# Kernel optimization log

Hardware: AMD Instinct MI355X
Metric: run time of the kernel (lower is better)

The kernel has to match this reference:

```python
import jax, jax.numpy as jnp
import numpy as np

EPS = 1e-5
GROUPS = 32


def _groupnorm(x, gamma, beta):
    B, C, H, W = x.shape
    xr = x.reshape(B, GROUPS, C // GROUPS, H, W)
    mu = xr.mean(axis=(2, 3, 4), keepdims=True)
    var = xr.var(axis=(2, 3, 4), keepdims=True)
    xn = ((xr - mu) * jax.lax.rsqrt(var + EPS)).reshape(B, C, H, W)
    return xn * gamma[None, :, None, None] + beta[None, :, None, None]


def _conv1x1(x, w, b):
    # x: [B,C,H,W], w: [Cout,Cin], b: [Cout]
    return jnp.einsum('bchw,oc->bohw', x, w) + b[None, :, None, None]


def setup_inputs() -> dict:
    key = jax.random.key(0)
    ks = jax.random.split(key, 11)
    B, C, H, W = 4, 64, 64, 64
    s = 0.05  # weight scale for well-conditioned softmax
    inp = {
        'x': jax.random.normal(ks[0], (B, C, H, W), jnp.float32),
        'gn_gamma': jnp.ones((C,), jnp.float32),
        'gn_beta': jnp.zeros((C,), jnp.float32),
        'wq': jax.random.normal(ks[1], (C, C), jnp.float32) * s,
        'bq': jnp.zeros((C,), jnp.float32),
        'wk': jax.random.normal(ks[2], (C, C), jnp.float32) * s,
        'bk': jnp.zeros((C,), jnp.float32),
        'wv': jax.random.normal(ks[3], (C, C), jnp.float32) * s,
        'bv': jnp.zeros((C,), jnp.float32),
        'wp': jax.random.normal(ks[4], (C, C), jnp.float32) * s,
        'bp': jnp.zeros((C,), jnp.float32),
    }
    return inp


def reference(x, gn_gamma, gn_beta, wq, bq, wk, bk, wv, bv, wp, bp):
    B, C, H, W = x.shape
    h = _groupnorm(x, gn_gamma, gn_beta)
    q = _conv1x1(h, wq, bq)
    k = _conv1x1(h, wk, bk)
    v = _conv1x1(h, wv, bv)
    # scores over all spatial positions: [B,H,W,H,W]
    scale = 1.0 / jnp.sqrt(jnp.asarray(C, x.dtype))
    w = jnp.einsum('bchw,bcHW->bhwHW', q, k) * scale
    w = jax.nn.softmax(w.reshape(B, H, W, H * W), axis=-1).reshape(B, H, W, H, W)
    h = jnp.einsum('bhwHW,bcHW->bchw', w, v)
    h = _conv1x1(h, wp, bp)
    return x + h
```

## Files before the change

kernel.cpp:

```cpp
#include <hip/hip_runtime.h>
#include <stdint.h>

#define Bn 4
#define Cn 64
#define Sn 4096
#define Gn 32

typedef float v4f __attribute__((ext_vector_type(4)));
typedef short v8s __attribute__((ext_vector_type(8)));
typedef short v4s __attribute__((ext_vector_type(4)));

#define MFMA16(a,b,c) __builtin_amdgcn_mfma_f32_16x16x32_bf16((a),(b),(c),0,0,0)

#define QSC 0.18033688011112042f

__device__ __forceinline__ float bf2f(uint16_t u){
  union { uint32_t i; float f; } x; x.i = ((uint32_t)u) << 16; return x.f;
}
__device__ __forceinline__ uint16_t f2bf(float f){
  union { float f; uint32_t i; } x; x.f = f;
  uint32_t r = x.i + 0x7fffu + ((x.i >> 16) & 1u);
  return (uint16_t)(r >> 16);
}
__device__ __forceinline__ uint32_t cvtpk(float a, float b){
  uint32_t r;
  asm("v_cvt_pk_bf16_f32 %0, %1, %2" : "=v"(r) : "v"(a), "v"(b));
  return r;
}

__global__ __launch_bounds__(256) void gn_stats(
    const float* __restrict__ x,
    const float* __restrict__ wq, const float* __restrict__ wk,
    const float* __restrict__ wv, const float* __restrict__ wp,
    float* __restrict__ stats, uint16_t* __restrict__ Wbf)
{
  const int tid = threadIdx.x;
  if (blockIdx.x >= 128) {
    const int m = blockIdx.x - 128;
    const float* src = (m == 0) ? wq : (m == 1) ? wk : (m == 2) ? wv : wp;
    const float sc  = (m == 0) ? QSC : 1.f;
    uint16_t* dst = Wbf + (m << 12);
    #pragma unroll
    for (int i = 0; i < 4; ++i) {
      const int e = (tid << 4) + (i << 2);
      float4 v = *(const float4*)(src + e);
      v4s o;
      o[0] = (short)f2bf(v.x*sc); o[1] = (short)f2bf(v.y*sc);
      o[2] = (short)f2bf(v.z*sc); o[3] = (short)f2bf(v.w*sc);
      *(v4s*)(dst + e) = o;
    }
    return;
  }
  const float* base = x + (size_t)blockIdx.x * 8192;
  float sum = 0.f, sq = 0.f;
  #pragma unroll
  for (int i = 0; i < 8; ++i) {
    float4 v = *(const float4*)(base + ((i << 8) + tid)*4);
    sum += v.x + v.y + v.z + v.w;
    sq  += v.x*v.x + v.y*v.y + v.z*v.z + v.w*v.w;
  }
  #pragma unroll
  for (int off = 1; off < 64; off <<= 1) {
    sum += __shfl_xor(sum, off);
    sq  += __shfl_xor(sq, off);
  }
  __shared__ float red[8];
  const int w = tid >> 6;
  if ((tid & 63) == 0) { red[w] = sum; red[4+w] = sq; }
  __syncthreads();
  if (tid == 0) {
    float s = red[0]+red[1]+red[2]+red[3];
    float q = red[4]+red[5]+red[6]+red[7];
    float mean = s * (1.f/8192.f);
    float var  = q * (1.f/8192.f) - mean*mean;
    stats[blockIdx.x]       = mean;
    stats[128 + blockIdx.x] = rsqrtf(fmaxf(var, 0.f) + 1e-5f);
  }
}

__global__ __launch_bounds__(256) void gn_qkv(
    const float* __restrict__ xg, const float* __restrict__ gamma,
    const float* __restrict__ beta, const uint16_t* __restrict__ Wbf,
    const float* __restrict__ bq, const float* __restrict__ bk,
    const float* __restrict__ bv,
    const float* __restrict__ stats,
    uint16_t* __restrict__ Qg, uint16_t* __restrict__ Kg, uint16_t* __restrict__ Vg)
{
  __shared__ uint16_t Hs[32*72];
  const int tid  = threadIdx.x;
  const int w    = tid >> 6;
  const int lane = tid & 63;
  const int l15  = lane & 15;
  const int quad = lane >> 4;
  const int b  = blockIdx.x >> 7;
  const int s0 = (blockIdx.x & 127) << 5;

  #pragma unroll
  for (int i = 0; i < 2; ++i) {
    const int idx  = (i << 8) + tid;
    const int c    = idx >> 3;
    const int col4 = idx & 7;
    const int g    = c >> 1;
    const float mean = stats[b*Gn + g];
    const float rstd = stats[128 + b*Gn + g];
    const float ga = gamma[c], be = beta[c];
    float4 v = *(const float4*)(xg + ((size_t)b*Cn + c)*Sn + s0 + (col4 << 2));
    const int sl = col4 << 2;
    Hs[(sl+0)*72 + c] = f2bf((v.x - mean)*rstd*ga + be);
    Hs[(sl+1)*72 + c] = f2bf((v.y - mean)*rstd*ga + be);
    Hs[(sl+2)*72 + c] = f2bf((v.z - mean)*rstd*ga + be);
    Hs[(sl+3)*72 + c] = f2bf((v.w - mean)*rstd*ga + be);
  }
  __syncthreads();

  v8s  wa0[3], wa1[3];
  float bias[3][4];
  #pragma unroll
  for (int t = 0; t < 3; ++t) {
    const int ot   = w*3 + t;
    const int wsel = ot >> 2;
    const int o16  = (ot & 3) << 4;
    const float* Bsel = (wsel == 0) ? bq : (wsel == 1) ? bk : bv;
    const float bsc   = (wsel == 0) ? QSC : 1.f;
    const uint16_t* Wr = Wbf + (wsel << 12) + (o16 + l15)*64 + (quad << 3);
    wa0[t] = *(const v8s*)(Wr);
    wa1[t] = *(const v8s*)(Wr + 32);
    #pragma unroll
    for (int r = 0; r < 4; ++r) bias[t][r] = Bsel[o16 + (quad << 2) + r]*bsc;
  }

  #pragma unroll
  for (int sub = 0; sub < 2; ++sub) {
    const uint16_t* hr = Hs + ((sub << 4) + l15)*72;
    v8s bh0 = *(const v8s*)(hr + (quad << 3));
    v8s bh1 = *(const v8s*)(hr + 32 + (quad << 3));
    const int s = s0 + (sub << 4) + l15;
    #pragma unroll
    for (int t = 0; t < 3; ++t) {
      const int ot   = w*3 + t;
      const int wsel = ot >> 2;
      const int o16  = (ot & 3) << 4;
      v4f d = (v4f){0.f,0.f,0.f,0.f};
      d = MFMA16(wa0[t], bh0, d);
      d = MFMA16(wa1[t], bh1, d);
      if (wsel <= 1) {
        v4s qv;
        #pragma unroll
        for (int r = 0; r < 4; ++r) qv[r] = (short)f2bf(d[r] + bias[t][r]);
        uint16_t* dst = (wsel == 0 ? Qg : Kg) + ((size_t)b*Sn + s)*64 + o16 + (quad << 2);
        *(v4s*)dst = qv;
      } else {
        #pragma unroll
        for (int r = 0; r < 4; ++r) {
          const int o = o16 + (quad << 2) + r;
          Vg[((size_t)b*Cn + o)*Sn + s] = f2bf(d[r] + bias[t][r]);
        }
      }
    }
  }
}

__global__ __launch_bounds__(256, 4) void attn_split(
    const uint16_t* __restrict__ Qg, const uint16_t* __restrict__ Kg,
    const uint16_t* __restrict__ Vg,
    uint16_t* __restrict__ Opart, float* __restrict__ lpart)
{
  __shared__ uint16_t Ks[2][64*72];
  __shared__ uint16_t Vs[2][64*72];

  const int tid  = threadIdx.x;
  const int w    = tid >> 6;
  const int lane = tid & 63;
  const int l15  = lane & 15;
  const int quad = lane >> 4;
  const int bx    = blockIdx.x;
  const int split = bx >> 7;
  const int bq    = (bx & 7)*16 + ((bx >> 3) & 15);
  const int b     = bq >> 5;
  const int qt    = bq & 31;
  const int slot  = (bq << 3) + split;
  const int i_base = qt << 7;
  const int j0     = split << 9;

  const uint16_t* Qb = Qg + ((size_t)b*Sn + i_base)*64;
  const uint16_t* Kb = Kg + (size_t)b*Sn*64;
  const uint16_t* Vb = Vg + (size_t)b*Cn*Sn;

  v8s qb[2][2];
  #pragma unroll
  for (int h = 0; h < 2; ++h) {
    const int row = (w << 5) + (h << 4) + l15;
    qb[h][0] = *(const v8s*)(Qb + row*64 + (quad << 3));
    qb[h][1] = *(const v8s*)(Qb + row*64 + 32 + (quad << 3));
  }

  const int e0 = tid << 3,         r0 = e0 >> 6, c0 = e0 & 63;
  const int e1 = (256 + tid) << 3, r1 = e1 >> 6, c1 = e1 & 63;

  *(v8s*)(Ks[0] + r0*72 + c0) = *(const v8s*)(Kb + j0*64 + e0);
  *(v8s*)(Ks[0] + r1*72 + c1) = *(const v8s*)(Kb + j0*64 + e1);
  *(v8s*)(Vs[0] + r0*72 + c0) = *(const v8s*)(Vb + (size_t)r0*Sn + j0 + c0);
  *(v8s*)(Vs[0] + r1*72 + c1) = *(const v8s*)(Vb + (size_t)r1*Sn + j0 + c1);

  const v8s ones8 = (v8s){0x3F80,0x3F80,0x3F80,0x3F80,0x3F80,0x3F80,0x3F80,0x3F80};

  v4f o_l[2];
  v4f o_acc[2][4];
  #pragma unroll
  for (int h = 0; h < 2; ++h) {
    o_l[h] = (v4f){0.f,0.f,0.f,0.f};
    #pragma unroll
    for (int nc = 0; nc < 4; ++nc) o_acc[h][nc] = (v4f){0.f,0.f,0.f,0.f};
  }

  __syncthreads();

  for (int kt = 0; kt < 8; ++kt) {
    const int cur = kt & 1;
    v8s kp0, kp1, vp0, vp1;
    if (kt < 7) {
      const int jb = j0 + ((kt + 1) << 6);
      kp0 = *(const v8s*)(Kb + jb*64 + e0);
      kp1 = *(const v8s*)(Kb + jb*64 + e1);
      vp0 = *(const v8s*)(Vb + (size_t)r0*Sn + jb + c0);
      vp1 = *(const v8s*)(Vb + (size_t)r1*Sn + jb + c1);
    }

    v8s ka[4][2];
    #pragma unroll
    for (int n = 0; n < 4; ++n) {
      const uint16_t* kr = Ks[cur] + ((n << 4) + l15)*72;
      ka[n][0] = *(const v8s*)(kr + (quad << 3));
      ka[n][1] = *(const v8s*)(kr + 32 + (quad << 3));
    }

    v8s pa[2][2];
    #pragma unroll
    for (int h = 0; h < 2; ++h) {
      v4f s[4];
      #pragma unroll
      for (int n = 0; n < 4; ++n) {
        v4f t = (v4f){0.f,0.f,0.f,0.f};
        t = MFMA16(ka[n][0], qb[h][0], t);
        t = MFMA16(ka[n][1], qb[h][1], t);
        s[n] = t;
      }
      union { v8s s8; uint32_t u[4]; } u0, u1;
      #pragma unroll
      for (int n = 0; n < 4; ++n) {
        const float p0 = __builtin_amdgcn_exp2f(s[n][0]);
        const float p1 = __builtin_amdgcn_exp2f(s[n][1]);
        const float p2 = __builtin_amdgcn_exp2f(s[n][2]);
        const float p3 = __builtin_amdgcn_exp2f(s[n][3]);
        const uint32_t w0 = cvtpk(p0, p1);
        const uint32_t w1 = cvtpk(p2, p3);
        if (n < 2) { u0.u[(n & 1)*2] = w0; u0.u[(n & 1)*2 + 1] = w1; }
        else       { u1.u[(n & 1)*2] = w0; u1.u[(n & 1)*2 + 1] = w1; }
      }
      pa[h][0] = u0.s8;
      pa[h][1] = u1.s8;
      o_l[h] = MFMA16(pa[h][0], ones8, o_l[h]);
      o_l[h] = MFMA16(pa[h][1], ones8, o_l[h]);
    }

    #pragma unroll
    for (int nc = 0; nc < 4; ++nc) {
      const uint16_t* vrow = Vs[cur] + ((nc << 4) + l15)*72;
      #pragma unroll
      for (int c = 0; c < 2; ++c) {
        union { v8s s8; v4s h4[2]; } vb;
        vb.h4[0] = *(const v4s*)(vrow + (c << 5) + (quad << 2));
        vb.h4[1] = *(const v4s*)(vrow + (c << 5) + 16 + (quad << 2));
        o_acc[0][nc] = MFMA16(pa[0][c], vb.s8, o_acc[0][nc]);
        o_acc[1][nc] = MFMA16(pa[1][c], vb.s8, o_acc[1][nc]);
      }
    }

    if (kt < 7) {
      const int nxt = cur ^ 1;
      *(v8s*)(Ks[nxt] + r0*72 + c0) = kp0;
      *(v8s*)(Ks[nxt] + r1*72 + c1) = kp1;
      *(v8s*)(Vs[nxt] + r0*72 + c0) = vp0;
      *(v8s*)(Vs[nxt] + r1*72 + c1) = vp1;
      __syncthreads();
    }
  }

  uint16_t* Ob = Opart + (size_t)slot*8192 + (size_t)(w << 5)*64;
  float*    lp = lpart + slot*128 + (w << 5);
  #pragma unroll
  for (int h = 0; h < 2; ++h)
    #pragma unroll
    for (int nc = 0; nc < 4; ++nc)
      #pragma unroll
      for (int r = 0; r < 4; ++r)
        Ob[((h << 4) + (quad << 2) + r)*64 + (nc << 4) + l15] = f2bf(o_acc[h][nc][r]);
  if (l15 == 0) {
    #pragma unroll
    for (int h = 0; h < 2; ++h)
      #pragma unroll
      for (int r = 0; r < 4; ++r)
        lp[(h << 4) + (quad << 2) + r] = o_l[h][r];
  }
}

__global__ __launch_bounds__(256) void proj_res(
    const uint16_t* __restrict__ Opart, const float* __restrict__ lpart,
    const uint16_t* __restrict__ Wbf, const float* __restrict__ bp,
    const float* __restrict__ xg, float* __restrict__ out)
{
  __shared__ uint16_t As[16*72];
  const int tid  = threadIdx.x;
  const int w    = tid >> 6;
  const int lane = tid & 63;
  const int l15  = lane & 15;
  const int quad = lane >> 4;

  const uint16_t* Wr = Wbf + (3 << 12) + ((w << 4) + l15)*64 + (quad << 3);
  const v8s a0 = *(const v8s*)(Wr);
  const v8s a1 = *(const v8s*)(Wr + 32);
  float bpv[4];
  #pragma unroll
  for (int r = 0; r < 4; ++r) bpv[r] = bp[(w << 4) + (quad << 2) + r];

  for (int rep = 0; rep < 4; ++rep) {
    const int vbx = (blockIdx.x << 2) + rep;
    const int b      = vbx >> 8;
    const int st     = vbx & 255;
    const int qt     = st >> 3;
    const int sub    = st & 7;
    const int s_base = st << 4;
    const uint16_t* po = Opart + (size_t)((b*32 + qt)*8)*8192 + (sub << 4)*64;
    const float*    pl = lpart + ((b*32 + qt)*8)*128 + (sub << 4);

    if (rep) __syncthreads();

    {
      const int e = tid << 2, row = tid >> 4, col = (tid & 15) << 2;
      float lsum = 0.f;
      #pragma unroll
      for (int sp = 0; sp < 8; ++sp) lsum += pl[sp*128 + row];
      const float linv = 1.f / lsum;
      float acc[4] = {0.f,0.f,0.f,0.f};
      #pragma unroll
      for (int sp = 0; sp < 8; ++sp) {
        v4s o = *(const v4s*)(po + (size_t)sp*8192 + e);
        #pragma unroll
        for (int j = 0; j < 4; ++j) acc[j] += bf2f((uint16_t)o[j]);
      }
      v4s a;
      #pragma unroll
      for (int j = 0; j < 4; ++j) a[j] = (short)f2bf(acc[j]*linv);
      *(v4s*)(As + row*72 + col) = a;
    }
    __syncthreads();

    v8s ba0 = *(const v8s*)(As + l15*72 + (quad << 3));
    v8s ba1 = *(const v8s*)(As + l15*72 + 32 + (quad << 3));
    v4f d = (v4f){0.f,0.f,0.f,0.f};
    d = MFMA16(a0, ba0, d);
    d = MFMA16(a1, ba1, d);
    const int s = s_base + l15;
    #pragma unroll
    for (int r = 0; r < 4; ++r) {
      const int o = (w << 4) + (quad << 2) + r;
      const size_t idx = ((size_t)b*Cn + o)*Sn + s;
      out[idx] = d[r] + bpv[r] + xg[idx];
    }
  }
}

extern "C" void kernel_launch(void* const* d_in, const int* in_sizes, int n_in,
                              void* d_out, int out_size, void* d_ws, size_t ws_size,
                              hipStream_t stream)
{
  const float* x     = (const float*)d_in[0];
  const float* gamma = (const float*)d_in[1];
  const float* beta  = (const float*)d_in[2];
  const float* wq    = (const float*)d_in[3];
  const float* bq    = (const float*)d_in[4];
  const float* wk    = (const float*)d_in[5];
  const float* bk    = (const float*)d_in[6];
  const float* wv    = (const float*)d_in[7];
  const float* bv    = (const float*)d_in[8];
  const float* wp    = (const float*)d_in[9];
  const float* bp    = (const float*)d_in[10];

  float*    stats = (float*)d_ws;
  uint16_t* Wbf   = (uint16_t*)d_ws + 2048;
  uint16_t* Qg    = (uint16_t*)d_ws + 32768;
  uint16_t* Kg    = Qg + (size_t)Bn*Sn*Cn;
  uint16_t* Vg    = Kg + (size_t)Bn*Sn*Cn;
  uint16_t* Opart = Vg + (size_t)Bn*Sn*Cn;
  float*    lpart = (float*)(Opart + (size_t)1024*8192);
  float*    outp  = (float*)d_out;

  gn_stats  <<<132, 256, 0, stream>>>(x, wq, wk, wv, wp, stats, Wbf);
  gn_qkv    <<<512, 256, 0, stream>>>(x, gamma, beta, Wbf, bq, bk, bv,
                                      stats, Qg, Kg, Vg);
  attn_split<<<1024, 256, 0, stream>>>(Qg, Kg, Vg, Opart, lpart);
  proj_res  <<<256, 256, 0, stream>>>(Opart, lpart, Wbf, bp, x, outp);
}
```

Measured before the change: 114.3 us.

## Double attention KV splits and halve KV tile to raise occupancy

The attention kernel now splits each query tile's keys into 16 chunks of 256 instead of 8 chunks of 512. It streams 32-key K/V tiles with smaller shared buffers and allows 8 blocks per CU, launching 2048 blocks. The projection kernel now reduces 16 partials instead of 8. The aim is more concurrent waves to hide latency. The cost is twice the partial-output write and read traffic and fewer MFMAs between barriers.

Result: slower. 291.0 us (+154.5%).

```diff
diff --git a/kernel.cpp b/kernel.cpp
--- a/kernel.cpp
+++ b/kernel.cpp
@@ -160,13 +160,13 @@
   }
 }
 
-__global__ __launch_bounds__(256, 4) void attn_split(
+__global__ __launch_bounds__(256, 8) void attn_split(
     const uint16_t* __restrict__ Qg, const uint16_t* __restrict__ Kg,
     const uint16_t* __restrict__ Vg,
     uint16_t* __restrict__ Opart, float* __restrict__ lpart)
 {
-  __shared__ uint16_t Ks[2][64*72];
-  __shared__ uint16_t Vs[2][64*72];
+  __shared__ uint16_t Ks[2][32*72];
+  __shared__ uint16_t Vs[2][64*40];
 
   const int tid  = threadIdx.x;
   const int w    = tid >> 6;
@@ -178,9 +178,9 @@
   const int bq    = (bx & 7)*16 + ((bx >> 3) & 15);
   const int b     = bq >> 5;
   const int qt    = bq & 31;
-  const int slot  = (bq << 3) + split;
+  const int slot  = (bq << 4) + split;
   const int i_base = qt << 7;
-  const int j0     = split << 9;
+  const int j0     = split << 8;
 
   const uint16_t* Qb = Qg + ((size_t)b*Sn + i_base)*64;
   const uint16_t* Kb = Kg + (size_t)b*Sn*64;
@@ -194,13 +194,11 @@
     qb[h][1] = *(const v8s*)(Qb + row*64 + 32 + (quad << 3));
   }
 
-  const int e0 = tid << 3,         r0 = e0 >> 6, c0 = e0 & 63;
-  const int e1 = (256 + tid) << 3, r1 = e1 >> 6, c1 = e1 & 63;
-
-  *(v8s*)(Ks[0] + r0*72 + c0) = *(const v8s*)(Kb + j0*64 + e0);
-  *(v8s*)(Ks[0] + r1*72 + c1) = *(const v8s*)(Kb + j0*64 + e1);
-  *(v8s*)(Vs[0] + r0*72 + c0) = *(const v8s*)(Vb + (size_t)r0*Sn + j0 + c0);
-  *(v8s*)(Vs[0] + r1*72 + c1) = *(const v8s*)(Vb + (size_t)r1*Sn + j0 + c1);
+  const int kr_ = tid >> 3, kc_ = (tid & 7) << 3;
+  const int vc_ = tid >> 2, vj_ = (tid & 3) << 3;
+
+  *(v8s*)(Ks[0] + kr_*72 + kc_) = *(const v8s*)(Kb + (size_t)(j0 + kr_)*64 + kc_);
+  *(v8s*)(Vs[0] + vc_*40 + vj_) = *(const v8s*)(Vb + (size_t)vc_*Sn + j0 + vj_);
 
   const v8s ones8 = (v8s){0x3F80,0x3F80,0x3F80,0x3F80,0x3F80,0x3F80,0x3F80,0x3F80};
 
@@ -217,71 +215,60 @@
 
   for (int kt = 0; kt < 8; ++kt) {
     const int cur = kt & 1;
-    v8s kp0, kp1, vp0, vp1;
+    v8s kp, vp;
     if (kt < 7) {
-      const int jb = j0 + ((kt + 1) << 6);
-      kp0 = *(const v8s*)(Kb + jb*64 + e0);
-      kp1 = *(const v8s*)(Kb + jb*64 + e1);
-      vp0 = *(const v8s*)(Vb + (size_t)r0*Sn + jb + c0);
-      vp1 = *(const v8s*)(Vb + (size_t)r1*Sn + jb + c1);
-    }
-
-    v8s ka[4][2];
-    #pragma unroll
-    for (int n = 0; n < 4; ++n) {
+      const int jb = j0 + ((kt + 1) << 5);
+      kp = *(const v8s*)(Kb + (size_t)(jb + kr_)*64 + kc_);
+      vp = *(const v8s*)(Vb + (size_t)vc_*Sn + jb + vj_);
+    }
+
+    v8s ka[2][2];
+    #pragma unroll
+    for (int n = 0; n < 2; ++n) {
       const uint16_t* kr = Ks[cur] + ((n << 4) + l15)*72;
       ka[n][0] = *(const v8s*)(kr + (quad << 3));
       ka[n][1] = *(const v8s*)(kr + 32 + (quad << 3));
     }
 
-    v8s pa[2][2];
+    v8s pa[2];
     #pragma unroll
     for (int h = 0; h < 2; ++h) {
-      v4f s[4];
-      #pragma unroll
-      for (int n = 0; n < 4; ++n) {
+      v4f s[2];
+      #pragma unroll
+      for (int n = 0; n < 2; ++n) {
         v4f t = (v4f){0.f,0.f,0.f,0.f};
         t = MFMA16(ka[n][0], qb[h][0], t);
         t = MFMA16(ka[n][1], qb[h][1], t);
         s[n] = t;
       }
-      union { v8s s8; uint32_t u[4]; } u0, u1;
-      #pragma unroll
-      for (int n = 0; n < 4; ++n) {
+      union { v8s s8; uint32_t u[4]; } u0;
+      #pragma unroll
+      for (int n = 0; n < 2; ++n) {
         const float p0 = __builtin_amdgcn_exp2f(s[n][0]);
         const float p1 = __builtin_amdgcn_exp2f(s[n][1]);
         const float p2 = __builtin_amdgcn_exp2f(s[n][2]);
         const float p3 = __builtin_amdgcn_exp2f(s[n][3]);
-        const uint32_t w0 = cvtpk(p0, p1);
-        const uint32_t w1 = cvtpk(p2, p3);
-        if (n < 2) { u0.u[(n & 1)*2] = w0; u0.u[(n & 1)*2 + 1] = w1; }
-        else       { u1.u[(n & 1)*2] = w0; u1.u[(n & 1)*2 + 1] = w1; }
+        u0.u[(n << 1)]     = cvtpk(p0, p1);
+        u0.u[(n << 1) + 1] = cvtpk(p2, p3);
       }
-      pa[h][0] = u0.s8;
-      pa[h][1] = u1.s8;
-      o_l[h] = MFMA16(pa[h][0], ones8, o_l[h]);
-      o_l[h] = MFMA16(pa[h][1], ones8, o_l[h]);
+      pa[h] = u0.s8;
+      o_l[h] = MFMA16(pa[h], ones8, o_l[h]);
     }
 
     #pragma unroll
     for (int nc = 0; nc < 4; ++nc) {
-      const uint16_t* vrow = Vs[cur] + ((nc << 4) + l15)*72;
-      #pragma unroll
-      for (int c = 0; c < 2; ++c) {
-        union { v8s s8; v4s h4[2]; } vb;
-        vb.h4[0] = *(const v4s*)(vrow + (c << 5) + (quad << 2));
-        vb.h4[1] = *(const v4s*)(vrow + (c << 5) + 16 + (quad << 2));
-        o_acc[0][nc] = MFMA16(pa[0][c], vb.s8, o_acc[0][nc]);
-        o_acc[1][nc] = MFMA16(pa[1][c], vb.s8, o_acc[1][nc]);
-      }
+      const uint16_t* vrow = Vs[cur] + ((nc << 4) + l15)*40;
+      union { v8s s8; v4s h4[2]; } vb;
+      vb.h4[0] = *(const v4s*)(vrow + (quad << 2));
+      vb.h4[1] = *(const v4s*)(vrow + 16 + (quad << 2));
+      o_acc[0][nc] = MFMA16(pa[0], vb.s8, o_acc[0][nc]);
+      o_acc[1][nc] = MFMA16(pa[1], vb.s8, o_acc[1][nc]);
     }
 
     if (kt < 7) {
       const int nxt = cur ^ 1;
-      *(v8s*)(Ks[nxt] + r0*72 + c0) = kp0;
-      *(v8s*)(Ks[nxt] + r1*72 + c1) = kp1;
-      *(v8s*)(Vs[nxt] + r0*72 + c0) = vp0;
-      *(v8s*)(Vs[nxt] + r1*72 + c1) = vp1;
+      *(v8s*)(Ks[nxt] + kr_*72 + kc_) = kp;
+      *(v8s*)(Vs[nxt] + vc_*40 + vj_) = vp;
       __syncthreads();
     }
   }
@@ -330,8 +317,8 @@
     const int qt     = st >> 3;
     const int sub    = st & 7;
     const int s_base = st << 4;
-    const uint16_t* po = Opart + (size_t)((b*32 + qt)*8)*8192 + (sub << 4)*64;
-    const float*    pl = lpart + ((b*32 + qt)*8)*128 + (sub << 4);
+    const uint16_t* po = Opart + (size_t)((b*32 + qt)*16)*8192 + (sub << 4)*64;
+    const float*    pl = lpart + ((b*32 + qt)*16)*128 + (sub << 4);
 
     if (rep) __syncthreads();
 
@@ -339,11 +326,11 @@
       const int e = tid << 2, row = tid >> 4, col = (tid & 15) << 2;
       float lsum = 0.f;
       #pragma unroll
-      for (int sp = 0; sp < 8; ++sp) lsum += pl[sp*128 + row];
+      for (int sp = 0; sp < 16; ++sp) lsum += pl[sp*128 + row];
       const float linv = 1.f / lsum;
       float acc[4] = {0.f,0.f,0.f,0.f};
       #pragma unroll
-      for (int sp = 0; sp < 8; ++sp) {
+      for (int sp = 0; sp < 16; ++sp) {
         v4s o = *(const v4s*)(po + (size_t)sp*8192 + e);
         #pragma unroll
         for (int j = 0; j < 4; ++j) acc[j] += bf2f((uint16_t)o[j]);
@@ -392,12 +379,12 @@
   uint16_t* Kg    = Qg + (size_t)Bn*Sn*Cn;
   uint16_t* Vg    = Kg + (size_t)Bn*Sn*Cn;
   uint16_t* Opart = Vg + (size_t)Bn*Sn*Cn;
-  float*    lpart = (float*)(Opart + (size_t)1024*8192);
+  float*    lpart = (float*)(Opart + (size_t)2048*8192);
   float*    outp  = (float*)d_out;
 
   gn_stats  <<<132, 256, 0, stream>>>(x, wq, wk, wv, wp, stats, Wbf);
   gn_qkv    <<<512, 256, 0, stream>>>(x, gamma, beta, Wbf, bq, bk, bv,
                                       stats, Qg, Kg, Vg);
-  attn_split<<<1024, 256, 0, stream>>>(Qg, Kg, Vg, Opart, lpart);
+  attn_split<<<2048, 256, 0, stream>>>(Qg, Kg, Vg, Opart, lpart);
   proj_res  <<<256, 256, 0, stream>>>(Opart, lpart, Wbf, bp, x, outp);
 }
```
